# Kernel optimization log

Hardware: AMD Instinct MI355X
Metric: run time of the kernel (lower is better)

Reference implementation:

```python
import jax, jax.numpy as jnp
import numpy as np
from jax import lax

TAU = 2.0
EPS = 1e-5
STEP = 10      # time steps
RATIO = 4     # TIM_ratio
HEADS = 16
SCALE = 0.25


@jax.custom_vjp
def _spike(v):
    return (v > 0.0).astype(v.dtype)

def _spike_fwd(v):
    return _spike(v), v

def _spike_bwd(v, g):
    alpha = 4.0  # sigmoid surrogate gradient
    s = jax.nn.sigmoid(alpha * v)
    return (g * alpha * s * (1.0 - s),)

_spike.defvjp(_spike_fwd, _spike_bwd)


def lif(x, vth=1.0):
    """LIF neuron over leading time dim: mem += (x-mem)/tau, fire, hard reset (detached)."""
    def step(mem, xt):
        mem = mem + (xt - mem) / TAU
        s = _spike(mem - vth)
        mem = mem * (1.0 - lax.stop_gradient(s))
        return mem, s
    _, out = lax.scan(step, jnp.zeros_like(x[0]), x)
    return out


def bn(x, p, axis):
    """Inference-mode batchnorm; p = stacked (gamma, beta, mean, var) along dim 0."""
    g, b, m, v = p
    sh = [1] * x.ndim
    sh[axis] = -1
    return (x - m.reshape(sh)) / jnp.sqrt(v.reshape(sh) + EPS) * g.reshape(sh) + b.reshape(sh)


def conv3d(x, w, groups=1):
    return lax.conv_general_dilated(
        x, w, window_strides=(1, 1, 1), padding=[(1, 1)] * 3,
        dimension_numbers=('NCDHW', 'OIDHW', 'NCDHW'),
        feature_group_count=groups)


def tim(x, up_w, bn1, down_w, bn2):
    # x: (T, B, C, H, W); conv3d treats T as channels, (C,H,W) as the volume
    T, B, C, H, W = x.shape
    y = conv3d(jnp.swapaxes(x, 0, 1), up_w)                      # (B, T*R, C, H, W)
    y = jnp.swapaxes(bn(y, bn1, 1), 0, 1)                        # (T*R, B, C, H, W)
    # MyNode reshapes (T*R*B, ...) into STEP time chunks of size R*B
    y = lif(y.reshape(STEP, -1, C, H, W)).reshape(T * RATIO, B, C, H, W)
    y = conv3d(jnp.swapaxes(y, 0, 1), down_w, groups=STEP)       # (B, T, C, H, W)
    y = jnp.swapaxes(bn(y, bn2, 1), 0, 1)                        # (T, B, C, H, W)
    return lif(y)


def ssa(x, q_w, q_bn, k_w, k_bn, v_w, v_bn, proj_w, proj_bn,
        tim_up_w, tim_bn1, tim_down_w, tim_bn2):
    T, B, C, H, W = x.shape
    N = H * W
    d = C // HEADS
    xf = x.reshape(T * B, C, N)

    def branch(w, bnp):
        y = bn(jnp.einsum('oc,bcn->bon', w, xf), bnp, 1).reshape(T, B, C, H, W)
        y = tim(y, tim_up_w, tim_bn1, tim_down_w, tim_bn2)       # binary spikes
        y = y.reshape(T, B, C, N).transpose(0, 1, 3, 2)          # (T, B, N, C)
        return y.reshape(T, B, N, HEADS, d).transpose(0, 1, 3, 2, 4)  # (T, B, h, N, d)

    q = branch(q_w, q_bn)
    k = branch(k_w, k_bn)
    v = branch(v_w, v_bn)
    attn = jnp.einsum('tbhnd,tbhmd->tbhnm', q, k)                # no softmax (spiking attn)
    o = jnp.einsum('tbhnm,tbhmd->tbhnd', attn, v) * SCALE
    o = o.transpose(0, 1, 2, 4, 3).reshape(T, B, C, N)           # merge (h, d) -> C
    o = lif(o, vth=0.5)                                          # attn_lif, threshold 0.5
    o = bn(jnp.einsum('oc,tbcn->tbon', proj_w, o), proj_bn, 2)   # 1x1 conv1d + BN1d
    return lif(o).reshape(T, B, C, H, W)


def mlp(x, fc1_w, fc1_b, fc1_bn, fc2_w, fc2_b, fc2_bn):
    T, B, C, H, W = x.shape
    y = jnp.einsum('oc,tbchw->tbohw', fc1_w, x) + fc1_b.reshape(1, 1, -1, 1, 1)
    y = lif(bn(y, fc1_bn, 2))
    y = jnp.einsum('oc,tbchw->tbohw', fc2_w, y) + fc2_b.reshape(1, 1, -1, 1, 1)
    return lif(bn(y, fc2_bn, 2))


def setup_inputs() -> dict:
    key = jax.random.key(0)
    ks = jax.random.split(key, 24)
    T, B, C, H, W = 10, 4, 256, 16, 16
    HID = 1024

    def bnp(k, c):
        k1, k2, k3, k4 = jax.random.split(k, 4)
        gamma = jax.random.uniform(k1, (c,), minval=0.5, maxval=1.5)
        beta = 0.1 * jax.random.normal(k2, (c,))
        mean = 0.1 * jax.random.normal(k3, (c,))
        var = jax.random.uniform(k4, (c,), minval=0.5, maxval=1.5)
        return jnp.stack([gamma, beta, mean, var]).astype(jnp.float32)

    inp = {
        'x': jax.random.normal(ks[0], (T, B, C, H, W), jnp.float32),
        'q_w': jax.random.normal(ks[1], (C, C)) / np.sqrt(C),
        'q_bn': bnp(ks[2], C),
        'k_w': jax.random.normal(ks[3], (C, C)) / np.sqrt(C),
        'k_bn': bnp(ks[4], C),
        'v_w': jax.random.normal(ks[5], (C, C)) / np.sqrt(C),
        'v_bn': bnp(ks[6], C),
        'proj_w': jax.random.normal(ks[7], (C, C)) / np.sqrt(C),
        'proj_bn': bnp(ks[8], C),
        'tim_up_w': jax.random.normal(ks[9], (STEP * RATIO, STEP, 3, 3, 3)) / np.sqrt(STEP * 27),
        'tim_bn1': bnp(ks[10], STEP * RATIO),
        'tim_down_w': jax.random.normal(ks[11], (STEP, RATIO, 3, 3, 3)) / np.sqrt(RATIO * 27),
        'tim_bn2': bnp(ks[12], STEP),
        'fc1_w': jax.random.normal(ks[13], (HID, C)) / np.sqrt(C),
        'fc1_b': 0.1 * jax.random.normal(ks[14], (HID,)),
        'fc1_bn': bnp(ks[15], HID),
        'fc2_w': jax.random.normal(ks[16], (C, HID)) / np.sqrt(HID),
        'fc2_b': 0.1 * jax.random.normal(ks[17], (C,)),
        'fc2_bn': bnp(ks[18], C),
    }
    return {k: v.astype(jnp.float32) for k, v in inp.items()}


def reference(x, q_w, q_bn, k_w, k_bn, v_w, v_bn, proj_w, proj_bn,
              tim_up_w, tim_bn1, tim_down_w, tim_bn2,
              fc1_w, fc1_b, fc1_bn, fc2_w, fc2_b, fc2_bn):
    h = x + ssa(x, q_w, q_bn, k_w, k_bn, v_w, v_bn, proj_w, proj_bn,
                tim_up_w, tim_bn1, tim_down_w, tim_bn2)
    return h + mlp(h, fc1_w, fc1_b, fc1_bn, fc2_w, fc2_b, fc2_bn)
```

## Files before the change

kernel.cpp:

```cpp
#include <hip/hip_runtime.h>
#include <cstdint>
#include <cstddef>

#define EPSF 1e-5f

typedef __attribute__((ext_vector_type(8))) short short8;
typedef __attribute__((ext_vector_type(4))) float f32x4;

__device__ __forceinline__ unsigned short bf16_rne(float f) {
    unsigned int u = __float_as_uint(f);
    u += 0x7FFFu + ((u >> 16) & 1u);
    return (unsigned short)(u >> 16);
}
__device__ __forceinline__ float bf16f(unsigned short h) {
    return __uint_as_float(((unsigned int)h) << 16);
}

__global__ __launch_bounds__(256) void split_pack_k(
    const float* __restrict__ W, unsigned short* __restrict__ P, int O, int K)
{
    int idx = blockIdx.x * 256 + threadIdx.x;
    int total = (O * K) >> 3;
    if (idx >= total) return;
    const int OT = O >> 4, KT = K >> 5;
    const int lane = idx & 63, tile = idx >> 6;
    const int kt = tile % KT, ot = tile / KT;
    const int quad = lane >> 4, l15 = lane & 15;
    const int row = ot * 16 + l15, col = kt * 32 + quad * 8;
    const size_t base = ((size_t)ot * KT + kt) * 512 + lane * 8;
    const size_t sOff = (size_t)OT * KT * 512;
#pragma unroll
    for (int j = 0; j < 8; ++j) {
        float v = W[(size_t)row * K + col + j];
        unsigned short h1 = bf16_rne(v);
        float r = v - bf16f(h1);
        unsigned short h2 = bf16_rne(r);
        float r2 = r - bf16f(h2);
        unsigned short h3 = bf16_rne(r2);
        P[base + j] = h1;
        P[sOff + base + j] = h2;
        P[2 * sOff + base + j] = h3;
    }
}

struct MArgs { const unsigned short* W[3]; float* Out[3]; const float* bn[3]; };

#define MM(AP, BQ)                                                            \
    {                                                                         \
        _Pragma("unroll") for (int mt = 0; mt < 2; ++mt)                      \
        _Pragma("unroll") for (int nt = 0; nt < 2; ++nt)                      \
            acc[mt][nt] = __builtin_amdgcn_mfma_f32_16x16x32_bf16(            \
                Af[AP][mt], Bf[BQ][nt], acc[mt][nt], 0, 0, 0);                \
    }

__global__ __launch_bounds__(256, 2) void mfma_gemm2(
    MArgs a, const float* __restrict__ X, const float* __restrict__ bias,
    int O, int K, int N, int splitB)
{
    const unsigned short* __restrict__ W = a.W[blockIdx.z];
    float* __restrict__ Out = a.Out[blockIdx.z];
    const float* __restrict__ bnp = a.bn[blockIdx.z];
    const int OT = O >> 4, KT = K >> 5;
    const size_t sOff = (size_t)OT * KT * 512;

    __shared__ float Bsm[2][32][65];

    const int slice  = blockIdx.y;
    const int tilesn = N >> 6;
    const int to = (blockIdx.x / tilesn) << 6;
    const int tn = (blockIdx.x % tilesn) << 6;
    const int tid = threadIdx.x;
    const int wid = tid >> 6, lane = tid & 63;
    const int quad = lane >> 4, l15 = lane & 15;
    const int wm = (wid >> 1) << 5, wn = (wid & 1) << 5;
    const int oti0 = (to + wm) >> 4;

    f32x4 acc[2][2];
#pragma unroll
    for (int mt = 0; mt < 2; ++mt)
#pragma unroll
        for (int nt = 0; nt < 2; ++nt)
#pragma unroll
            for (int r = 0; r < 4; ++r) acc[mt][nt][r] = 0.0f;

    const float* Xs = X + (size_t)slice * K * N;
    const int nn = tid & 63, r0 = tid >> 6;

    float breg[8];
#pragma unroll
    for (int it = 0; it < 8; ++it)
        breg[it] = Xs[(size_t)(it * 4 + r0) * N + tn + nn];
#pragma unroll
    for (int it = 0; it < 8; ++it)
        Bsm[0][it * 4 + r0][nn] = breg[it];
    __syncthreads();

    for (int kt = 0; kt < KT; ++kt) {
        const int cur = kt & 1;
        if (kt + 1 < KT) {
#pragma unroll
            for (int it = 0; it < 8; ++it)
                breg[it] = Xs[(size_t)((kt + 1) * 32 + it * 4 + r0) * N + tn + nn];
        }
        short8 Af[3][2];
#pragma unroll
        for (int mt = 0; mt < 2; ++mt) {
            const size_t fb = ((size_t)(oti0 + mt) * KT + kt) * 512 + lane * 8;
            Af[0][mt] = *(const short8*)(W + fb);
            Af[1][mt] = *(const short8*)(W + sOff + fb);
            Af[2][mt] = *(const short8*)(W + 2 * sOff + fb);
        }
        short8 Bf[3][2];
#pragma unroll
        for (int nt = 0; nt < 2; ++nt) {
            const int bc = wn + (nt << 4) + l15;
            if (splitB == 3) {
#pragma unroll
                for (int j = 0; j < 8; ++j) {
                    float v = Bsm[cur][(quad << 3) + j][bc];
                    unsigned short h1 = bf16_rne(v);
                    float r = v - bf16f(h1);
                    unsigned short h2 = bf16_rne(r);
                    float r2 = r - bf16f(h2);
                    Bf[0][nt][j] = (short)h1;
                    Bf[1][nt][j] = (short)h2;
                    Bf[2][nt][j] = (short)bf16_rne(r2);
                }
            } else {
#pragma unroll
                for (int j = 0; j < 8; ++j)
                    Bf[0][nt][j] = (short)bf16_rne(Bsm[cur][(quad << 3) + j][bc]);
            }
        }

        if (splitB == 3) {
            MM(0, 0) MM(0, 1) MM(1, 0) MM(0, 2) MM(1, 1) MM(2, 0)
        } else {
            MM(0, 0) MM(1, 0) MM(2, 0)
        }

        if (kt + 1 < KT) {
            const int nxt = cur ^ 1;
#pragma unroll
            for (int it = 0; it < 8; ++it)
                Bsm[nxt][it * 4 + r0][nn] = breg[it];
        }
        __syncthreads();
    }

    float* Op = Out + (size_t)slice * O * N;
#pragma unroll
    for (int mt = 0; mt < 2; ++mt) {
#pragma unroll
        for (int r = 0; r < 4; ++r) {
            const int o = to + wm + (mt << 4) + (quad << 2) + r;
            float g = bnp[o], bb = bnp[O + o], m = bnp[2 * O + o], vv = bnp[3 * O + o];
            float sq = sqrtf(vv + EPSF);
            float bs = bias ? bias[o] : 0.0f;
#pragma unroll
            for (int nt = 0; nt < 2; ++nt) {
                const int n = tn + wn + (nt << 4) + l15;
                float val = acc[mt][nt][r] + bs;
                Op[(size_t)o * N + n] = (val - m) / sq * g + bb;
            }
        }
    }
}

__global__ __launch_bounds__(256) void wt_k(
    const float* __restrict__ up_w, float* __restrict__ WT)
{
    int idx = blockIdx.x * 256 + threadIdx.x;
    if (idx >= 12960) return;
    int slot = idx % 48, tq = idx / 48;
    int g = slot / 12, u = slot % 12;
    float v = 0.0f;
    if (u < 10) v = up_w[(4 * u + g) * 270 + tq];
    WT[idx] = v;
}

__global__ __launch_bounds__(256, 8) void tim_up4(
    const float* __restrict__ Y, const float* __restrict__ WT,
    const float* __restrict__ bn1, float* __restrict__ SPK)
{
    __shared__ float smem[5 * 3 * 200];
    const int c = blockIdx.x;
    const int b = blockIdx.y >> 1, half = blockIdx.y & 1;
    const int tid = threadIdx.x;
    const int lane = tid & 63;
    const int g = __builtin_amdgcn_readfirstlane(tid >> 6);
    const int hb2 = (lane >> 4) << 1;
    const int wc = lane & 15;

    float acc[2][10];
#pragma unroll
    for (int i = 0; i < 2; ++i)
#pragma unroll
        for (int u = 0; u < 10; ++u) acc[i][u] = 0.0f;

#pragma unroll 1
    for (int ph = 0; ph < 2; ++ph) {
        __syncthreads();
        for (int idx = tid; idx < 3000; idx += 256) {
            int t = ph * 5 + idx / 600, rem = idx % 600;
            int cc = rem / 200, p = rem % 200;
            int rr = p / 20, col = p % 20;
            int h = half * 8 + rr - 1, ww = col - 1;
            int cs = c + cc - 1;
            float v = 0.0f;
            if (cs >= 0 && cs < 256 && h >= 0 && h < 16 && ww >= 0 && ww < 16)
                v = Y[((t * 4 + b) * 256 + cs) * 256 + h * 16 + ww];
            smem[idx] = v;
        }
        __syncthreads();

#pragma unroll 1
        for (int tt = 0; tt < 5; ++tt) {
            const int t = ph * 5 + tt;
#pragma unroll
            for (int kd = 0; kd < 3; ++kd) {
                const float* sp = &smem[tt * 600 + kd * 200 + hb2 * 20 + wc];
                float vr[4][3];
#pragma unroll
                for (int r = 0; r < 4; ++r)
#pragma unroll
                    for (int kc = 0; kc < 3; ++kc)
                        vr[r][kc] = sp[r * 20 + kc];
#pragma unroll
                for (int q = 0; q < 9; ++q) {
                    const int kh = q / 3, kw = q % 3;
                    const float4* wp =
                        (const float4*)&WT[(t * 27 + kd * 9 + q) * 48 + g * 12];
                    float4 w0 = wp[0], w1 = wp[1];
                    float4 w2 = wp[2];
                    float wr[10] = {w0.x, w0.y, w0.z, w0.w, w1.x,
                                    w1.y, w1.z, w1.w, w2.x, w2.y};
#pragma unroll
                    for (int u = 0; u < 10; ++u)
#pragma unroll
                        for (int i = 0; i < 2; ++i)
                            acc[i][u] = fmaf(wr[u], vr[i + kh][kw], acc[i][u]);
                }
            }
        }
    }

#pragma unroll
    for (int i = 0; i < 2; ++i) {
        const int h = half * 8 + hb2 + i;
        float mem = 0.0f;
#pragma unroll
        for (int s = 0; s < 10; ++s) {
            const int uc = 4 * s + g;
            float ga = bn1[uc], be = bn1[40 + uc], mu = bn1[80 + uc], va = bn1[120 + uc];
            float xv = (acc[i][s] - mu) / sqrtf(va + EPSF) * ga + be;
            mem += (xv - mem) * 0.5f;
            float spk = mem > 1.0f ? 1.0f : 0.0f;
            SPK[(((size_t)b * 40 + uc) * 256 + c) * 256 + h * 16 + wc] = spk;
            mem = spk > 0.0f ? 0.0f : mem;
        }
    }
}

__global__ __launch_bounds__(256) void tim_down_pre(
    const float* __restrict__ SPK, const float* __restrict__ w,
    const float* __restrict__ bn2, float* __restrict__ PreY)
{
    __shared__ float smem[4 * 3 * 324];
    const int c = blockIdx.x, b = blockIdx.y, t = blockIdx.z;
    const int tid = threadIdx.x;
    for (int idx = tid; idx < 3888; idx += 256) {
        int r = idx / 972, rem = idx % 972;
        int cc = rem / 324, p = rem % 324;
        int hh = p / 18 - 1, ww = p % 18 - 1;
        int cs = c + cc - 1;
        float v = 0.0f;
        if (cs >= 0 && cs < 256 && hh >= 0 && hh < 16 && ww >= 0 && ww < 16)
            v = SPK[(((size_t)b * 40 + 4 * t + r) * 256 + cs) * 256 + hh * 16 + ww];
        smem[idx] = v;
    }
    __syncthreads();
    const int h = tid >> 4, wq = tid & 15;
    float a = 0.0f;
#pragma unroll
    for (int r = 0; r < 4; ++r)
#pragma unroll
        for (int kd = 0; kd < 3; ++kd) {
            const float* wp = w + ((t * 4 + r) * 3 + kd) * 9;
#pragma unroll
            for (int kh = 0; kh < 3; ++kh)
#pragma unroll
                for (int kw = 0; kw < 3; ++kw)
                    a = fmaf(wp[kh * 3 + kw],
                             smem[r * 972 + kd * 324 + (h + kh) * 18 + (wq + kw)], a);
        }
    a = (a - bn2[20 + t]) / sqrtf(bn2[30 + t] + EPSF) * bn2[t] + bn2[10 + t];
    PreY[((t * 4 + b) * 256 + c) * 256 + tid] = a;
}

__global__ __launch_bounds__(256) void lif_down(
    const float* __restrict__ PreY, float* __restrict__ S)
{
    const int idx = blockIdx.x * 256 + threadIdx.x;
    float mem = 0.0f;
    for (int t = 0; t < 10; ++t) {
        float v = PreY[t * 262144 + idx];
        mem += (v - mem) * 0.5f;
        float spk = mem > 1.0f ? 1.0f : 0.0f;
        S[t * 262144 + idx] = spk;
        mem = spk > 0.0f ? 0.0f : mem;
    }
}

__global__ __launch_bounds__(256) void ktv_k(
    const float* __restrict__ SK, const float* __restrict__ SV,
    float* __restrict__ KTV)
{
    __shared__ float ks[16 * 257], vs[16 * 257];
    const int bi = blockIdx.x;
    const int t = bi >> 6, b = (bi >> 4) & 3, hd = bi & 15;
    const int tid = threadIdx.x;
    for (int i = tid; i < 4096; i += 256) {
        int row = i >> 8, col = i & 255;
        ks[row * 257 + col] = SK[((t * 4 + b) * 256 + hd * 16 + row) * 256 + col];
        vs[row * 257 + col] = SV[((t * 4 + b) * 256 + hd * 16 + row) * 256 + col];
    }
    __syncthreads();
    const int j = tid >> 4, j2 = tid & 15;
    float a0 = 0.0f, a1 = 0.0f, a2 = 0.0f, a3 = 0.0f;
#pragma unroll 4
    for (int n = 0; n < 256; n += 4) {
        a0 = fmaf(ks[j * 257 + n + 0], vs[j2 * 257 + n + 0], a0);
        a1 = fmaf(ks[j * 257 + n + 1], vs[j2 * 257 + n + 1], a1);
        a2 = fmaf(ks[j * 257 + n + 2], vs[j2 * 257 + n + 2], a2);
        a3 = fmaf(ks[j * 257 + n + 3], vs[j2 * 257 + n + 3], a3);
    }
    KTV[((t * 4 + b) * 16 + hd) * 256 + tid] = (a0 + a1) + (a2 + a3);
}

__global__ __launch_bounds__(256) void attn_k(
    const float* __restrict__ SQ, const float* __restrict__ KTV,
    float* __restrict__ OSPK)
{
    __shared__ float kt[2560];
    __shared__ float qs[16 * 17];
    const int x = blockIdx.x;
    const int b = x >> 8, hd = (x >> 4) & 15, ng = x & 15;
    const int tid = threadIdx.x;
    const int j2 = tid >> 4, nl = tid & 15;
    const int n = ng * 16 + nl;
    for (int i = tid; i < 2560; i += 256) {
        int t = i >> 8;
        kt[i] = KTV[((t * 4 + b) * 16 + hd) * 256 + (i & 255)];
    }
    float mem = 0.0f;
    for (int t = 0; t < 10; ++t) {
        __syncthreads();
        qs[nl * 17 + j2] = SQ[((t * 4 + b) * 256 + hd * 16 + j2) * 256 + n];
        __syncthreads();
        float a = 0.0f;
#pragma unroll
        for (int j = 0; j < 16; ++j)
            a = fmaf(qs[nl * 17 + j], kt[t * 256 + j * 16 + j2], a);
        a *= 0.25f;
        mem += (a - mem) * 0.5f;
        float spk = mem > 0.5f ? 1.0f : 0.0f;
        OSPK[((t * 4 + b) * 256 + hd * 16 + j2) * 256 + n] = spk;
        mem = spk > 0.0f ? 0.0f : mem;
    }
}

__global__ __launch_bounds__(256) void ssa_lif_res(
    const float* __restrict__ P, const float* __restrict__ x,
    float* __restrict__ H)
{
    const int idx = blockIdx.x * 256 + threadIdx.x;
    float mem = 0.0f;
    for (int t = 0; t < 10; ++t) {
        float v = P[t * 262144 + idx];
        mem += (v - mem) * 0.5f;
        float spk = mem > 1.0f ? 1.0f : 0.0f;
        H[t * 262144 + idx] = x[t * 262144 + idx] + spk;
        mem = spk > 0.0f ? 0.0f : mem;
    }
}

__global__ __launch_bounds__(256) void lif_ip(float* __restrict__ A)
{
    const int idx = blockIdx.x * 256 + threadIdx.x;
    float mem = 0.0f;
    for (int t = 0; t < 10; ++t) {
        float v = A[t * 1048576 + idx];
        mem += (v - mem) * 0.5f;
        float spk = mem > 1.0f ? 1.0f : 0.0f;
        A[t * 1048576 + idx] = spk;
        mem = spk > 0.0f ? 0.0f : mem;
    }
}

__global__ __launch_bounds__(256) void final_k(
    const float* __restrict__ P, const float* __restrict__ H,
    float* __restrict__ out)
{
    const int idx = blockIdx.x * 256 + threadIdx.x;
    float mem = 0.0f;
    for (int t = 0; t < 10; ++t) {
        float v = P[t * 262144 + idx];
        mem += (v - mem) * 0.5f;
        float spk = mem > 1.0f ? 1.0f : 0.0f;
        out[t * 262144 + idx] = H[t * 262144 + idx] + spk;
        mem = spk > 0.0f ? 0.0f : mem;
    }
}

extern "C" void kernel_launch(void* const* d_in, const int* in_sizes, int n_in,
                              void* d_out, int out_size, void* d_ws, size_t ws_size,
                              hipStream_t stream)
{
    const float* x        = (const float*)d_in[0];
    const float* q_w      = (const float*)d_in[1];
    const float* q_bn     = (const float*)d_in[2];
    const float* k_w      = (const float*)d_in[3];
    const float* k_bn     = (const float*)d_in[4];
    const float* v_w      = (const float*)d_in[5];
    const float* v_bn     = (const float*)d_in[6];
    const float* proj_w   = (const float*)d_in[7];
    const float* proj_bn  = (const float*)d_in[8];
    const float* up_w     = (const float*)d_in[9];
    const float* bn1      = (const float*)d_in[10];
    const float* down_w   = (const float*)d_in[11];
    const float* bn2      = (const float*)d_in[12];
    const float* fc1_w    = (const float*)d_in[13];
    const float* fc1_b    = (const float*)d_in[14];
    const float* fc1_bn   = (const float*)d_in[15];
    const float* fc2_w    = (const float*)d_in[16];
    const float* fc2_b    = (const float*)d_in[17];
    const float* fc2_bn   = (const float*)d_in[18];

    float* ws   = (float*)d_ws;
    float* Y    = ws;
    float* ASPK = Y + 2621440;
    float* SQ   = ASPK + 10485760;
    float* SK   = SQ + 2621440;
    float* SV   = SK + 2621440;
    float* KTV  = SV + 2621440;
    float* WT   = KTV;

    float* Yb[3] = {Y, SK, SV};
    float* Sb[3] = {SQ, SK, SV};

    unsigned short* qs_s = (unsigned short*)ASPK;
    unsigned short* ks_s = qs_s + 196608;
    unsigned short* vs_s = qs_s + 393216;

    wt_k<<<51, 256, 0, stream>>>(up_w, WT);
    split_pack_k<<<32, 256, 0, stream>>>(q_w, qs_s, 256, 256);
    split_pack_k<<<32, 256, 0, stream>>>(k_w, ks_s, 256, 256);
    split_pack_k<<<32, 256, 0, stream>>>(v_w, vs_s, 256, 256);

    MArgs qkv;
    qkv.W[0] = qs_s;  qkv.W[1] = ks_s;  qkv.W[2] = vs_s;
    qkv.Out[0] = Yb[0]; qkv.Out[1] = Yb[1]; qkv.Out[2] = Yb[2];
    qkv.bn[0] = q_bn; qkv.bn[1] = k_bn; qkv.bn[2] = v_bn;
    mfma_gemm2<<<dim3(16, 40, 3), 256, 0, stream>>>(qkv, x, nullptr, 256, 256, 256, 3);

    for (int br = 0; br < 3; ++br) {
        tim_up4<<<dim3(256, 8), 256, 0, stream>>>(Yb[br], WT, bn1, ASPK);
        tim_down_pre<<<dim3(256, 4, 10), 256, 0, stream>>>(ASPK, down_w, bn2, Y);
        lif_down<<<1024, 256, 0, stream>>>(Y, Sb[br]);
    }

    ktv_k<<<640, 256, 0, stream>>>(SK, SV, KTV);
    attn_k<<<1024, 256, 0, stream>>>(SQ, KTV, Y);

    unsigned short* pj_s = (unsigned short*)ASPK;
    split_pack_k<<<32, 256, 0, stream>>>(proj_w, pj_s, 256, 256);
    MArgs gp; gp.W[0] = gp.W[1] = gp.W[2] = pj_s;
    gp.Out[0] = gp.Out[1] = gp.Out[2] = SQ;
    gp.bn[0] = gp.bn[1] = gp.bn[2] = proj_bn;
    mfma_gemm2<<<dim3(16, 40, 1), 256, 0, stream>>>(gp, Y, nullptr, 256, 256, 256, 1);
    ssa_lif_res<<<1024, 256, 0, stream>>>(SQ, x, SV);

    unsigned short* f1_s = (unsigned short*)Y;
    split_pack_k<<<128, 256, 0, stream>>>(fc1_w, f1_s, 1024, 256);
    MArgs g1; g1.W[0] = g1.W[1] = g1.W[2] = f1_s;
    g1.Out[0] = g1.Out[1] = g1.Out[2] = ASPK;
    g1.bn[0] = g1.bn[1] = g1.bn[2] = fc1_bn;
    mfma_gemm2<<<dim3(64, 40, 1), 256, 0, stream>>>(g1, SV, fc1_b, 1024, 256, 256, 3);
    lif_ip<<<4096, 256, 0, stream>>>(ASPK);

    unsigned short* f2_s = (unsigned short*)Y;
    split_pack_k<<<128, 256, 0, stream>>>(fc2_w, f2_s, 256, 1024);
    MArgs g2; g2.W[0] = g2.W[1] = g2.W[2] = f2_s;
    g2.Out[0] = g2.Out[1] = g2.Out[2] = SK;
    g2.bn[0] = g2.bn[1] = g2.bn[2] = fc2_bn;
    mfma_gemm2<<<dim3(16, 40, 1), 256, 0, stream>>>(g2, ASPK, fc2_b, 256, 1024, 256, 1);
    final_k<<<1024, 256, 0, stream>>>(SK, SV, (float*)d_out);
}
```

Baseline: 780.9 us.

## Pre-pack activation operand into split-bf16 MFMA fragments for 3-way split GEMMs

Adds a bpack kernel that converts the fp32 activation matrix into three bf16 split components, stored in MFMA fragment order. A new GEMM kernel then loads both A and B fragments straight from global memory, with no shared-memory staging and no per-tile conversion. This is used for the QKV and fc1 GEMMs, and the three weight-pack launches are merged into one. The aim is to cut the redundant per-block split arithmetic and the LDS traffic. The cost is an extra pass that writes three bf16 copies of the activation. Occupancy hints also change: gemm3 asks for 4 blocks per unit and tim_up4 goes from 8 to 6.

```diff
diff --git a/kernel.cpp b/kernel.cpp
--- a/kernel.cpp
+++ b/kernel.cpp
@@ -16,12 +16,10 @@
     return __uint_as_float(((unsigned int)h) << 16);
 }
 
-__global__ __launch_bounds__(256) void split_pack_k(
-    const float* __restrict__ W, unsigned short* __restrict__ P, int O, int K)
-{
-    int idx = blockIdx.x * 256 + threadIdx.x;
-    int total = (O * K) >> 3;
-    if (idx >= total) return;
+__device__ __forceinline__ void split_pack_body(
+    const float* __restrict__ W, unsigned short* __restrict__ P,
+    int O, int K, int idx)
+{
     const int OT = O >> 4, KT = K >> 5;
     const int lane = idx & 63, tile = idx >> 6;
     const int kt = tile % KT, ot = tile / KT;
@@ -36,10 +34,54 @@
         float r = v - bf16f(h1);
         unsigned short h2 = bf16_rne(r);
         float r2 = r - bf16f(h2);
-        unsigned short h3 = bf16_rne(r2);
         P[base + j] = h1;
         P[sOff + base + j] = h2;
-        P[2 * sOff + base + j] = h3;
+        P[2 * sOff + base + j] = bf16_rne(r2);
+    }
+}
+
+__global__ __launch_bounds__(256) void split_pack_k(
+    const float* __restrict__ W, unsigned short* __restrict__ P, int O, int K)
+{
+    int idx = blockIdx.x * 256 + threadIdx.x;
+    if (idx >= (O * K) >> 3) return;
+    split_pack_body(W, P, O, K, idx);
+}
+
+struct SplitArgs { const float* W[3]; unsigned short* P[3]; };
+__global__ __launch_bounds__(256) void split_pack3_k(SplitArgs sa, int O, int K)
+{
+    int idx = blockIdx.x * 256 + threadIdx.x;
+    if (idx >= (O * K) >> 3) return;
+    split_pack_body(sa.W[blockIdx.y], sa.P[blockIdx.y], O, K, idx);
+}
+
+__global__ __launch_bounds__(256) void bpack_k(
+    const float* __restrict__ B, unsigned short* __restrict__ BP,
+    int K, int N, int S)
+{
+    const int KT = K >> 5, NT16 = N >> 4;
+    int idx = blockIdx.x * 256 + threadIdx.x;
+    if (idx >= S * NT16 * KT * 64) return;
+    const int lane = idx & 63;
+    int tile = idx >> 6;
+    const int kt = tile % KT; tile /= KT;
+    const int n16 = tile % NT16; const int s = tile / NT16;
+    const int quad = lane >> 4, l15 = lane & 15;
+    const size_t base = (size_t)idx * 8;
+    const size_t sOff = (size_t)S * NT16 * KT * 512;
+    const float* src = B + (size_t)s * K * N + (size_t)(kt * 32 + quad * 8) * N
+                         + n16 * 16 + l15;
+#pragma unroll
+    for (int j = 0; j < 8; ++j) {
+        float v = src[(size_t)j * N];
+        unsigned short h1 = bf16_rne(v);
+        float r = v - bf16f(h1);
+        unsigned short h2 = bf16_rne(r);
+        float r2 = r - bf16f(h2);
+        BP[base + j] = h1;
+        BP[sOff + base + j] = h2;
+        BP[2 * sOff + base + j] = bf16_rne(r2);
     }
 }
 
@@ -53,17 +95,16 @@
                 Af[AP][mt], Bf[BQ][nt], acc[mt][nt], 0, 0, 0);                \
     }
 
-__global__ __launch_bounds__(256, 2) void mfma_gemm2(
-    MArgs a, const float* __restrict__ X, const float* __restrict__ bias,
-    int O, int K, int N, int splitB)
+__global__ __launch_bounds__(256, 4) void mfma_gemm3(
+    MArgs a, const unsigned short* __restrict__ BP,
+    const float* __restrict__ bias, int O, int K, int N)
 {
     const unsigned short* __restrict__ W = a.W[blockIdx.z];
     float* __restrict__ Out = a.Out[blockIdx.z];
     const float* __restrict__ bnp = a.bn[blockIdx.z];
-    const int OT = O >> 4, KT = K >> 5;
-    const size_t sOff = (size_t)OT * KT * 512;
-
-    __shared__ float Bsm[2][32][65];
+    const int OT = O >> 4, KT = K >> 5, NT16 = N >> 4;
+    const size_t sA = (size_t)OT * KT * 512;
+    const size_t sB = (size_t)gridDim.y * NT16 * KT * 512;
 
     const int slice  = blockIdx.y;
     const int tilesn = N >> 6;
@@ -74,6 +115,76 @@
     const int quad = lane >> 4, l15 = lane & 15;
     const int wm = (wid >> 1) << 5, wn = (wid & 1) << 5;
     const int oti0 = (to + wm) >> 4;
+    const int n160 = (tn + wn) >> 4;
+
+    f32x4 acc[2][2];
+#pragma unroll
+    for (int mt = 0; mt < 2; ++mt)
+#pragma unroll
+        for (int nt = 0; nt < 2; ++nt)
+#pragma unroll
+            for (int r = 0; r < 4; ++r) acc[mt][nt][r] = 0.0f;
+
+    for (int kt = 0; kt < KT; ++kt) {
+        short8 Af[3][2], Bf[3][2];
+#pragma unroll
+        for (int mt = 0; mt < 2; ++mt) {
+            const size_t fa = ((size_t)(oti0 + mt) * KT + kt) * 512 + lane * 8;
+            Af[0][mt] = *(const short8*)(W + fa);
+            Af[1][mt] = *(const short8*)(W + sA + fa);
+            Af[2][mt] = *(const short8*)(W + 2 * sA + fa);
+        }
+#pragma unroll
+        for (int nt = 0; nt < 2; ++nt) {
+            const size_t fb =
+                (((size_t)slice * NT16 + n160 + nt) * KT + kt) * 512 + lane * 8;
+            Bf[0][nt] = *(const short8*)(BP + fb);
+            Bf[1][nt] = *(const short8*)(BP + sB + fb);
+            Bf[2][nt] = *(const short8*)(BP + 2 * sB + fb);
+        }
+        MM(0, 0) MM(0, 1) MM(1, 0) MM(0, 2) MM(1, 1) MM(2, 0)
+    }
+
+    float* Op = Out + (size_t)slice * O * N;
+#pragma unroll
+    for (int mt = 0; mt < 2; ++mt) {
+#pragma unroll
+        for (int r = 0; r < 4; ++r) {
+            const int o = to + wm + (mt << 4) + (quad << 2) + r;
+            float g = bnp[o], bb = bnp[O + o], m = bnp[2 * O + o], vv = bnp[3 * O + o];
+            float sq = sqrtf(vv + EPSF);
+            float bs = bias ? bias[o] : 0.0f;
+#pragma unroll
+            for (int nt = 0; nt < 2; ++nt) {
+                const int n = tn + wn + (nt << 4) + l15;
+                float val = acc[mt][nt][r] + bs;
+                Op[(size_t)o * N + n] = (val - m) / sq * g + bb;
+            }
+        }
+    }
+}
+
+__global__ __launch_bounds__(256, 2) void mfma_gemm2(
+    MArgs a, const float* __restrict__ X, const float* __restrict__ bias,
+    int O, int K, int N)
+{
+    const unsigned short* __restrict__ W = a.W[blockIdx.z];
+    float* __restrict__ Out = a.Out[blockIdx.z];
+    const float* __restrict__ bnp = a.bn[blockIdx.z];
+    const int OT = O >> 4, KT = K >> 5;
+    const size_t sOff = (size_t)OT * KT * 512;
+
+    __shared__ float Bsm[2][32][65];
+
+    const int slice  = blockIdx.y;
+    const int tilesn = N >> 6;
+    const int to = (blockIdx.x / tilesn) << 6;
+    const int tn = (blockIdx.x % tilesn) << 6;
+    const int tid = threadIdx.x;
+    const int wid = tid >> 6, lane = tid & 63;
+    const int quad = lane >> 4, l15 = lane & 15;
+    const int wm = (wid >> 1) << 5, wn = (wid & 1) << 5;
+    const int oti0 = (to + wm) >> 4;
 
     f32x4 acc[2][2];
 #pragma unroll
@@ -110,35 +221,15 @@
             Af[1][mt] = *(const short8*)(W + sOff + fb);
             Af[2][mt] = *(const short8*)(W + 2 * sOff + fb);
         }
-        short8 Bf[3][2];
+        short8 Bf[1][2];
 #pragma unroll
         for (int nt = 0; nt < 2; ++nt) {
             const int bc = wn + (nt << 4) + l15;
-            if (splitB == 3) {
-#pragma unroll
-                for (int j = 0; j < 8; ++j) {
-                    float v = Bsm[cur][(quad << 3) + j][bc];
-                    unsigned short h1 = bf16_rne(v);
-                    float r = v - bf16f(h1);
-                    unsigned short h2 = bf16_rne(r);
-                    float r2 = r - bf16f(h2);
-                    Bf[0][nt][j] = (short)h1;
-                    Bf[1][nt][j] = (short)h2;
-                    Bf[2][nt][j] = (short)bf16_rne(r2);
-                }
-            } else {
-#pragma unroll
-                for (int j = 0; j < 8; ++j)
-                    Bf[0][nt][j] = (short)bf16_rne(Bsm[cur][(quad << 3) + j][bc]);
-            }
-        }
-
-        if (splitB == 3) {
-            MM(0, 0) MM(0, 1) MM(1, 0) MM(0, 2) MM(1, 1) MM(2, 0)
-        } else {
-            MM(0, 0) MM(1, 0) MM(2, 0)
-        }
-
+#pragma unroll
+            for (int j = 0; j < 8; ++j)
+                Bf[0][nt][j] = (short)bf16_rne(Bsm[cur][(quad << 3) + j][bc]);
+        }
+        MM(0, 0) MM(1, 0) MM(2, 0)
         if (kt + 1 < KT) {
             const int nxt = cur ^ 1;
 #pragma unroll
@@ -179,7 +270,7 @@
     WT[idx] = v;
 }
 
-__global__ __launch_bounds__(256, 8) void tim_up4(
+__global__ __launch_bounds__(256, 6) void tim_up4(
     const float* __restrict__ Y, const float* __restrict__ WT,
     const float* __restrict__ bn1, float* __restrict__ SPK)
 {
@@ -452,17 +543,20 @@
     unsigned short* qs_s = (unsigned short*)ASPK;
     unsigned short* ks_s = qs_s + 196608;
     unsigned short* vs_s = qs_s + 393216;
+    unsigned short* xp_s = qs_s + 589824;
 
     wt_k<<<51, 256, 0, stream>>>(up_w, WT);
-    split_pack_k<<<32, 256, 0, stream>>>(q_w, qs_s, 256, 256);
-    split_pack_k<<<32, 256, 0, stream>>>(k_w, ks_s, 256, 256);
-    split_pack_k<<<32, 256, 0, stream>>>(v_w, vs_s, 256, 256);
+    SplitArgs sa;
+    sa.W[0] = q_w; sa.W[1] = k_w; sa.W[2] = v_w;
+    sa.P[0] = qs_s; sa.P[1] = ks_s; sa.P[2] = vs_s;
+    split_pack3_k<<<dim3(32, 3), 256, 0, stream>>>(sa, 256, 256);
+    bpack_k<<<1280, 256, 0, stream>>>(x, xp_s, 256, 256, 40);
 
     MArgs qkv;
     qkv.W[0] = qs_s;  qkv.W[1] = ks_s;  qkv.W[2] = vs_s;
     qkv.Out[0] = Yb[0]; qkv.Out[1] = Yb[1]; qkv.Out[2] = Yb[2];
     qkv.bn[0] = q_bn; qkv.bn[1] = k_bn; qkv.bn[2] = v_bn;
-    mfma_gemm2<<<dim3(16, 40, 3), 256, 0, stream>>>(qkv, x, nullptr, 256, 256, 256, 3);
+    mfma_gemm3<<<dim3(16, 40, 3), 256, 0, stream>>>(qkv, xp_s, nullptr, 256, 256, 256);
 
     for (int br = 0; br < 3; ++br) {
         tim_up4<<<dim3(256, 8), 256, 0, stream>>>(Yb[br], WT, bn1, ASPK);
@@ -478,15 +572,17 @@
     MArgs gp; gp.W[0] = gp.W[1] = gp.W[2] = pj_s;
     gp.Out[0] = gp.Out[1] = gp.Out[2] = SQ;
     gp.bn[0] = gp.bn[1] = gp.bn[2] = proj_bn;
-    mfma_gemm2<<<dim3(16, 40, 1), 256, 0, stream>>>(gp, Y, nullptr, 256, 256, 256, 1);
+    mfma_gemm2<<<dim3(16, 40, 1), 256, 0, stream>>>(gp, Y, nullptr, 256, 256, 256);
     ssa_lif_res<<<1024, 256, 0, stream>>>(SQ, x, SV);
 
+    unsigned short* f1b = (unsigned short*)SQ;
+    bpack_k<<<1280, 256, 0, stream>>>(SV, f1b, 256, 256, 40);
     unsigned short* f1_s = (unsigned short*)Y;
     split_pack_k<<<128, 256, 0, stream>>>(fc1_w, f1_s, 1024, 256);
     MArgs g1; g1.W[0] = g1.W[1] = g1.W[2] = f1_s;
     g1.Out[0] = g1.Out[1] = g1.Out[2] = ASPK;
     g1.bn[0] = g1.bn[1] = g1.bn[2] = fc1_bn;
-    mfma_gemm2<<<dim3(64, 40, 1), 256, 0, stream>>>(g1, SV, fc1_b, 1024, 256, 256, 3);
+    mfma_gemm3<<<dim3(64, 40, 1), 256, 0, stream>>>(g1, f1b, fc1_b, 1024, 256, 256);
     lif_ip<<<4096, 256, 0, stream>>>(ASPK);
 
     unsigned short* f2_s = (unsigned short*)Y;
@@ -494,6 +590,6 @@
     MArgs g2; g2.W[0] = g2.W[1] = g2.W[2] = f2_s;
     g2.Out[0] = g2.Out[1] = g2.Out[2] = SK;
     g2.bn[0] = g2.bn[1] = g2.bn[2] = fc2_bn;
-    mfma_gemm2<<<dim3(16, 40, 1), 256, 0, stream>>>(g2, ASPK, fc2_b, 256, 1024, 256, 1);
+    mfma_gemm2<<<dim3(16, 40, 1), 256, 0, stream>>>(g2, ASPK, fc2_b, 256, 1024, 256);
     final_k<<<1024, 256, 0, stream>>>(SK, SV, (float*)d_out);
 }
```

Measured after the change: 749.9 us. -4.0%, faster.
